# Optimization experiments

Measured on AMD Instinct MI355X. Metric: run time of the kernel, lower is better.

The kernel has to match this reference:

```python
import jax, jax.numpy as jnp
import numpy as np

H = 64
N_G, E_G = 30000, 60000
N_LG, E_LG = 60000, 60000


def setup_inputs() -> dict:
    key = jax.random.key(0)
    ks = jax.random.split(key, 30)
    rn = lambda k, s, sc=0.05: jax.random.normal(k, s, jnp.float32) * sc
    return {
        "gx": jax.random.normal(ks[0], (N_G, 20), jnp.float32),
        "g_edge_index": jax.random.randint(ks[1], (2, E_G), 0, N_G, jnp.int32),
        "g_edge_attr": jax.random.uniform(ks[2], (E_G, 4), dtype=jnp.float32),
        "lgx": jax.random.normal(ks[3], (N_LG, 5), jnp.float32),
        "lg_edge_index": jax.random.randint(ks[4], (2, E_LG), 0, N_LG, jnp.int32),
        "lg_edge_attr": jax.random.uniform(ks[5], (E_LG, 1), dtype=jnp.float32),
        "adduct": jax.random.normal(ks[6], (3,), jnp.float32),
        "lin0_w": rn(ks[7], (20, H)), "lin0_b": rn(ks[8], (H,)),
        "g_nn_w1": rn(ks[9], (4, H)), "g_nn_b1": rn(ks[10], (H,)),
        "g_nn_w2": rn(ks[11], (H, H * H), 0.01), "g_nn_b2": rn(ks[12], (H * H,), 0.01),
        "g_root": rn(ks[13], (H, H)), "g_bias": rn(ks[14], (H,)),
        "lin0_lg_w": rn(ks[15], (5, H)), "lin0_lg_b": rn(ks[16], (H,)),
        "lg_nn_w1": rn(ks[17], (1, H)), "lg_nn_b1": rn(ks[18], (H,)),
        "lg_nn_w2": rn(ks[19], (H, H * H), 0.01), "lg_nn_b2": rn(ks[20], (H * H,), 0.01),
        "lg_root": rn(ks[21], (H, H)), "lg_bias": rn(ks[22], (H,)),
        "bott_w": rn(ks[23], (H + H + 3, 384)), "bott_b": rn(ks[24], (384,)),
        "lin1_w": rn(ks[25], (384, 384)), "lin1_b": rn(ks[26], (384,)),
        "lin2_w": rn(ks[27], (384, 1)), "lin2_b": rn(ks[28], (1,)),
    }


def _ecc_branch(x_in, edge_index, edge_attr, w1, b1, w2, b2, root, bias, n_iters, num_nodes):
    """N iterations of NNConv(aggr='mean') + ReLU, then sum pool over nodes."""
    src, tgt = edge_index[0], edge_index[1]  # source->target flow (PyG default)
    # edge MLP -> per-edge [in, out] weight (edge_attr is loop-invariant, compute once)
    W = (jax.nn.relu(edge_attr @ w1 + b1) @ w2 + b2).reshape(-1, H, H)  # [E, H, H]
    cnt = jnp.maximum(
        jax.ops.segment_sum(jnp.ones((tgt.shape[0],), x_in.dtype), tgt, num_segments=num_nodes),
        1.0,
    )
    x = x_in
    for _ in range(n_iters):
        msg = jnp.einsum('ei,eio->eo', x[src], W)  # gather + batched matvec
        agg = jax.ops.segment_sum(msg, tgt, num_segments=num_nodes) / cnt[:, None]  # scatter-mean
        x = jax.nn.relu(x @ root + agg + bias)  # root transform + bias (NNConv defaults)
    return x.sum(axis=0)  # sum pooling -> [H]


def reference(gx, g_edge_index, g_edge_attr, lgx, lg_edge_index, lg_edge_attr, adduct,
              lin0_w, lin0_b, g_nn_w1, g_nn_b1, g_nn_w2, g_nn_b2, g_root, g_bias,
              lin0_lg_w, lin0_lg_b, lg_nn_w1, lg_nn_b1, lg_nn_w2, lg_nn_b2, lg_root, lg_bias,
              bott_w, bott_b, lin1_w, lin1_b, lin2_w, lin2_b):
    out_g = _ecc_branch(jax.nn.relu(gx @ lin0_w + lin0_b), g_edge_index, g_edge_attr,
                        g_nn_w1, g_nn_b1, g_nn_w2, g_nn_b2, g_root, g_bias, 3, N_G)
    out_lg = _ecc_branch(jax.nn.relu(lgx @ lin0_lg_w + lin0_lg_b), lg_edge_index, lg_edge_attr,
                         lg_nn_w1, lg_nn_b1, lg_nn_w2, lg_nn_b2, lg_root, lg_bias, 3, N_LG)
    out = jnp.concatenate([out_g, out_lg, adduct], axis=-1)  # [131]
    out = jax.nn.relu(out @ bott_w + bott_b)
    for _ in range(6):
        out = jax.nn.relu(out @ lin1_w + lin1_b)
    return out @ lin2_w + lin2_b  # [1]
```

## Files before the change

### kernel.cpp

```cpp
#include <hip/hip_runtime.h>

typedef unsigned short u16;
using short8_t  = __attribute__((ext_vector_type(8)))  short;
using float16_t = __attribute__((ext_vector_type(16))) float;
using float2v   = __attribute__((ext_vector_type(2)))  float;

#define NKT 260
#define DEG_CAP 32

__device__ __forceinline__ float bf2f(u16 b) { return __uint_as_float(((unsigned)b) << 16); }
__device__ __forceinline__ u16 f2bf(float f) {
  unsigned u = __float_as_uint(f);
  return (u16)((u + 0x7fffu + ((u >> 16) & 1u)) >> 16);
}

union U8 { short8_t s; uint4 v; unsigned u[4]; };

__device__ __forceinline__ short8_t scale8r(U8 xr, float2v h2) {
  U8 out;
  #pragma unroll
  for (int p = 0; p < 4; ++p) {
    float2v r;
    r[0] = __uint_as_float(xr.u[p] << 16);
    r[1] = __uint_as_float(xr.u[p] & 0xffff0000u);
    r = r * h2;
    out.u[p] = __builtin_amdgcn_perm(__float_as_uint(r[1]), __float_as_uint(r[0]), 0x07060302);
  }
  return out.s;
}

template<int IN>
__device__ __forceinline__ void affine_body(
    const float* __restrict__ Xin, const float* __restrict__ W, const float* __restrict__ Bv,
    u16* __restrict__ Xout, int N, int gid)
{
  int n = gid >> 6, o = gid & 63;
  if (n >= N) return;
  float acc = Bv[o];
  #pragma unroll
  for (int i = 0; i < IN; ++i)
    acc = fmaf(Xin[n * IN + i], W[i * 64 + o], acc);
  Xout[gid] = f2bf(fmaxf(acc, 0.f));
}

__global__ __launch_bounds__(256) void affine_all_kernel(
    const float* __restrict__ gx, const float* __restrict__ l0w, const float* __restrict__ l0b, u16* __restrict__ xg,
    const float* __restrict__ lgx, const float* __restrict__ llw, const float* __restrict__ llb, u16* __restrict__ xl,
    const float* __restrict__ gea, const float* __restrict__ gw1, const float* __restrict__ gb1, u16* __restrict__ hg,
    const float* __restrict__ lea, const float* __restrict__ lw1, const float* __restrict__ lb1, u16* __restrict__ hl,
    int B0, int B1, int B2, int B3, int NG, int NLG, int EG, int ELG,
    int* __restrict__ zero_ptr, int NZ)
{
  int b = blockIdx.x, t = threadIdx.x;
  if (b < B0)       affine_body<20>(gx, l0w, l0b, xg, NG, b * 256 + t);
  else if (b < B1)  affine_body<5>(lgx, llw, llb, xl, NLG, (b - B0) * 256 + t);
  else if (b < B2)  affine_body<4>(gea, gw1, gb1, hg, EG, (b - B1) * 256 + t);
  else if (b < B3)  affine_body<1>(lea, lw1, lb1, hl, ELG, (b - B2) * 256 + t);
  else {
    int idx = (b - B3) * 256 + t;
    if (idx < NZ) zero_ptr[idx] = 0;
  }
}

__device__ __forceinline__ void bpack_body(
    const float* __restrict__ w2, const float* __restrict__ b2, u16* __restrict__ Bp, int gid)
{
  if (gid >= NKT * 128) return;
  int lane = gid & 63;
  int nt = (gid >> 6) & 1;
  int kt = gid >> 7;
  int o = nt * 32 + (lane & 31);
  int kbase = kt * 16 + (lane >> 5) * 8;
  u16 vals[8];
  #pragma unroll
  for (int j = 0; j < 8; ++j) {
    int k = kbase + j;
    vals[j] = f2bf((k < 4096) ? w2[(k >> 6) * 4096 + (k & 63) * 64 + o]
                              : b2[(k - 4096) * 64 + o]);
  }
  uint4 pack;
  pack.x = (unsigned)vals[0] | ((unsigned)vals[1] << 16);
  pack.y = (unsigned)vals[2] | ((unsigned)vals[3] << 16);
  pack.z = (unsigned)vals[4] | ((unsigned)vals[5] << 16);
  pack.w = (unsigned)vals[6] | ((unsigned)vals[7] << 16);
  *(uint4*)(Bp + (size_t)gid * 8) = pack;
}

__device__ __forceinline__ void rootpack_body(const float* __restrict__ root, u16* __restrict__ Rp, int gid)
{
  if (gid >= 512) return;
  int lane = gid & 63;
  int nt = (gid >> 6) & 1;
  int kt = gid >> 7;
  int o = nt * 32 + (lane & 31);
  int kbase = kt * 16 + (lane >> 5) * 8;
  u16 vals[8];
  #pragma unroll
  for (int j = 0; j < 8; ++j) vals[j] = f2bf(root[(kbase + j) * 64 + o]);
  uint4 pack;
  pack.x = (unsigned)vals[0] | ((unsigned)vals[1] << 16);
  pack.y = (unsigned)vals[2] | ((unsigned)vals[3] << 16);
  pack.z = (unsigned)vals[4] | ((unsigned)vals[5] << 16);
  pack.w = (unsigned)vals[6] | ((unsigned)vals[7] << 16);
  *(uint4*)(Rp + (size_t)gid * 8) = pack;
}

__global__ __launch_bounds__(256) void pack_all_kernel(
    const float* __restrict__ gw2, const float* __restrict__ gb2, u16* __restrict__ bpg,
    const float* __restrict__ lw2, const float* __restrict__ lb2, u16* __restrict__ bpl,
    const float* __restrict__ groot, u16* __restrict__ rpg,
    const float* __restrict__ lroot, u16* __restrict__ rpl)
{
  int b = blockIdx.x, t = threadIdx.x;
  if (b < 130)       bpack_body(gw2, gb2, bpg, b * 256 + t);
  else if (b < 260)  bpack_body(lw2, lb2, bpl, (b - 130) * 256 + t);
  else if (b < 262)  rootpack_body(groot, rpg, (b - 260) * 256 + t);
  else               rootpack_body(lroot, rpl, (b - 262) * 256 + t);
}

__device__ __forceinline__ void hist_body(
    const int* __restrict__ eidx, int* __restrict__ cnt, int* __restrict__ elist, int E, int e)
{
  if (e < E) {
    int tg = eidx[E + e];
    int pos = atomicAdd(cnt + tg, 1);
    if (pos < DEG_CAP) elist[(size_t)tg * DEG_CAP + pos] = e;
  }
}

__global__ __launch_bounds__(256) void hist_kernel(
    const int* __restrict__ eig, int* __restrict__ cg, int* __restrict__ elg, int Eg, int nbg,
    const int* __restrict__ eil, int* __restrict__ cl, int* __restrict__ ell, int El)
{
  int b = blockIdx.x, t = threadIdx.x;
  if (b < nbg) hist_body(eig, cg, elg, Eg, b * 256 + t);
  else         hist_body(eil, cl, ell, El, (b - nbg) * 256 + t);
}

__global__ __launch_bounds__(256, 2) void msg_gemm_kernel(
    const u16* __restrict__ Xg, const u16* __restrict__ Hg, const u16* __restrict__ Bg,
    const int* __restrict__ eig, u16* __restrict__ Mg, int Eg, int nbg,
    const u16* __restrict__ Xl, const u16* __restrict__ Hl, const u16* __restrict__ Bl,
    const int* __restrict__ eil, u16* __restrict__ Ml, int El)
{
  __shared__ __align__(16) u16 sB[4][8192];

  const int b = blockIdx.x;
  const u16 *X, *Hh, *Bp; const int* eidx; u16* msg; int E, e0;
  if (b < nbg) { X = Xg; Hh = Hg; Bp = Bg; eidx = eig; msg = Mg; E = Eg; e0 = b * 256; }
  else         { X = Xl; Hh = Hl; Bp = Bl; eidx = eil; msg = Ml; E = El; e0 = (b - nbg) * 256; }

  const int t = threadIdx.x;
  const int lane = t & 63;
  const int wid = t >> 6;
  const int ml = lane & 31;
  const int q  = lane >> 5;

  #pragma unroll
  for (int c0 = 0; c0 < 3; ++c0) {
    const u16* src = Bp + (size_t)c0 * 8192 + (size_t)wid * 2048 + (size_t)lane * 8;
    u16* dst = &sB[c0][wid * 2048];
    #pragma unroll
    for (int d = 0; d < 4; ++d)
      __builtin_amdgcn_global_load_lds((const __attribute__((address_space(1))) void*)(src + d * 512),
                                       (__attribute__((address_space(3))) void*)(dst + d * 512), 16, 0, 0);
  }

  const int ea  = e0 + wid * 64 + ml;
  const int eb  = ea + 32;
  const int eac = ea < E ? ea : E - 1;
  const int ebc = eb < E ? eb : E - 1;
  const int sa  = eidx[eac], sb = eidx[ebc];

  U8 xra[4], xrb[4];
  {
    const u16* xpa = X + (size_t)sa * 64 + q * 8;
    const u16* xpb = X + (size_t)sb * 64 + q * 8;
    #pragma unroll
    for (int s = 0; s < 4; ++s) {
      xra[s].v = *(const uint4*)(xpa + s * 16);
      xrb[s].v = *(const uint4*)(xpb + s * 16);
    }
  }

  const uint4* ha4 = (const uint4*)(Hh + (size_t)eac * 64);
  const uint4* hb4 = (const uint4*)(Hh + (size_t)ebc * 64);
  uint4 hc0 = ha4[0], hn0 = ha4[1];
  uint4 hc1 = hb4[0], hn1 = hb4[1];

  float16_t acc00, acc01, acc10, acc11;
  #pragma unroll
  for (int i = 0; i < 16; ++i) { acc00[i] = 0.f; acc01[i] = 0.f; acc10[i] = 0.f; acc11[i] = 0.f; }

  const u16* bsrc = Bp + (size_t)3 * 8192 + (size_t)wid * 2048 + (size_t)lane * 8;

  const short8_t* sb8 = (const short8_t*)&sB[0][0];

  asm volatile("s_waitcnt vmcnt(0)" ::: "memory");
  __builtin_amdgcn_sched_barrier(0);
  __builtin_amdgcn_s_barrier();

  for (int g = 0; g < 8; ++g) {
    #pragma unroll
    for (int cc = 0; cc < 4; ++cc) {
      {
        #pragma unroll
        for (int d = 0; d < 4; ++d)
          __builtin_amdgcn_global_load_lds((const __attribute__((address_space(1))) void*)(bsrc + d * 512),
                                           (__attribute__((address_space(3))) void*)(&sB[(cc + 3) & 3][wid * 2048] + d * 512), 16, 0, 0);
        bsrc += 8192;
      }
      unsigned w0 = ((const unsigned*)&hc0)[cc];
      unsigned w1 = ((const unsigned*)&hc1)[cc];
      const int sbase = (cc & 3) * 1024;
      #pragma unroll
      for (int hh = 0; hh < 2; ++hh) {
        float2v h20, h21;
        h20[0] = h20[1] = bf2f((u16)(hh ? (w0 >> 16) : (w0 & 0xffffu)));
        h21[0] = h21[1] = bf2f((u16)(hh ? (w1 >> 16) : (w1 & 0xffffu)));
        #pragma unroll
        for (int tt = 0; tt < 4; ++tt) {
          short8_t b0 = sb8[sbase + (hh * 4 + tt) * 128 + lane];
          short8_t b1 = sb8[sbase + (hh * 4 + tt) * 128 + 64 + lane];
          short8_t a0 = scale8r(xra[tt], h20);
          short8_t a1 = scale8r(xrb[tt], h21);
          acc00 = __builtin_amdgcn_mfma_f32_32x32x16_bf16(a0, b0, acc00, 0, 0, 0);
          acc01 = __builtin_amdgcn_mfma_f32_32x32x16_bf16(a0, b1, acc01, 0, 0, 0);
          acc10 = __builtin_amdgcn_mfma_f32_32x32x16_bf16(a1, b0, acc10, 0, 0, 0);
          acc11 = __builtin_amdgcn_mfma_f32_32x32x16_bf16(a1, b1, acc11, 0, 0, 0);
        }
      }
      asm volatile("s_waitcnt lgkmcnt(0)" ::: "memory");
      asm volatile("s_waitcnt vmcnt(8)" ::: "memory");
      __builtin_amdgcn_sched_barrier(0);
      __builtin_amdgcn_s_barrier();
    }
    hc0 = hn0; hc1 = hn1;
    if (g < 6) { hn0 = ha4[g + 2]; hn1 = hb4[g + 2]; }
  }

  {
    float2v h2; h2[0] = 1.0f; h2[1] = 1.0f;
    #pragma unroll
    for (int tt = 0; tt < 4; ++tt) {
      short8_t b0 = sb8[tt * 128 + lane];
      short8_t b1 = sb8[tt * 128 + 64 + lane];
      short8_t a0 = scale8r(xra[tt], h2);
      short8_t a1 = scale8r(xrb[tt], h2);
      acc00 = __builtin_amdgcn_mfma_f32_32x32x16_bf16(a0, b0, acc00, 0, 0, 0);
      acc01 = __builtin_amdgcn_mfma_f32_32x32x16_bf16(a0, b1, acc01, 0, 0, 0);
      acc10 = __builtin_amdgcn_mfma_f32_32x32x16_bf16(a1, b0, acc10, 0, 0, 0);
      acc11 = __builtin_amdgcn_mfma_f32_32x32x16_bf16(a1, b1, acc11, 0, 0, 0);
    }
  }

  #pragma unroll
  for (int reg = 0; reg < 16; ++reg) {
    int row = (reg & 3) + 8 * (reg >> 2) + 4 * q;
    int e1 = e0 + wid * 64 + row;
    int e2 = e1 + 32;
    if (e1 < E) {
      msg[(size_t)e1 * 64 + ml]      = f2bf(acc00[reg]);
      msg[(size_t)e1 * 64 + 32 + ml] = f2bf(acc01[reg]);
    }
    if (e2 < E) {
      msg[(size_t)e2 * 64 + ml]      = f2bf(acc10[reg]);
      msg[(size_t)e2 * 64 + 32 + ml] = f2bf(acc11[reg]);
    }
  }
}

__global__ __launch_bounds__(256, 4) void update_kernel(
    const u16* __restrict__ Xig, const u16* __restrict__ Mgg, const int* __restrict__ cg,
    const int* __restrict__ elg, const u16* __restrict__ rpg, const float* __restrict__ bg,
    u16* __restrict__ Xog, int Ng, int nbg,
    const u16* __restrict__ Xil, const u16* __restrict__ Mgl, const int* __restrict__ cl,
    const int* __restrict__ ell, const u16* __restrict__ rpl, const float* __restrict__ bl,
    u16* __restrict__ Xol, int Nl)
{
  const int b = blockIdx.x;
  const u16 *Xin, *rootp, *msg; const float *bias; const int *cnt, *elist;
  u16* Xout; int N, n0;
  if (b < nbg) { Xin=Xig; msg=Mgg; cnt=cg; elist=elg; rootp=rpg; bias=bg; Xout=Xog; N=Ng; n0=b*128; }
  else         { Xin=Xil; msg=Mgl; cnt=cl; elist=ell; rootp=rpl; bias=bl; Xout=Xol; N=Nl; n0=(b-nbg)*128; }

  const int t = threadIdx.x;
  const int lane = t & 63;
  const int wid = t >> 6;
  const int ml = lane & 31;
  const int q  = lane >> 5;
  const int nbase = n0 + wid * 32;

  const int na = nbase + ml;
  const int nac = na < N ? na : N - 1;

  U8 xr[4];
  {
    const u16* xp = Xin + (size_t)nac * 64 + q * 8;
    #pragma unroll
    for (int s = 0; s < 4; ++s) xr[s].v = *(const uint4*)(xp + s * 16);
  }
  U8 rp[8];
  {
    const uint4* rpv = (const uint4*)rootp;
    #pragma unroll
    for (int i = 0; i < 8; ++i) rp[i].v = rpv[i * 64 + lane];
  }
  const float bias0 = bias[ml], bias1 = bias[32 + ml];

  float16_t acc0, acc1;
  #pragma unroll
  for (int i = 0; i < 16; ++i) { acc0[i] = 0.f; acc1[i] = 0.f; }
  #pragma unroll
  for (int kt = 0; kt < 4; ++kt) {
    acc0 = __builtin_amdgcn_mfma_f32_32x32x16_bf16(xr[kt].s, rp[kt * 2 + 0].s, acc0, 0, 0, 0);
    acc1 = __builtin_amdgcn_mfma_f32_32x32x16_bf16(xr[kt].s, rp[kt * 2 + 1].s, acc1, 0, 0, 0);
  }

  #pragma unroll
  for (int reg = 0; reg < 16; ++reg) {
    int row = (reg & 3) + 8 * (reg >> 2) + 4 * q;
    int nn = nbase + row;
    if (nn < N) {
      int c = cnt[nn];
      int cc = c < DEG_CAP ? c : DEG_CAP;
      const int* ep = elist + (size_t)nn * DEG_CAP;
      float a0 = 0.f, a1 = 0.f;
      int j = 0;
      for (; j + 4 <= cc; j += 4) {
        int e0i = ep[j], e1i = ep[j + 1], e2i = ep[j + 2], e3i = ep[j + 3];
        u16 m00 = msg[(size_t)e0i * 64 + ml], m01 = msg[(size_t)e0i * 64 + 32 + ml];
        u16 m10 = msg[(size_t)e1i * 64 + ml], m11 = msg[(size_t)e1i * 64 + 32 + ml];
        u16 m20 = msg[(size_t)e2i * 64 + ml], m21 = msg[(size_t)e2i * 64 + 32 + ml];
        u16 m30 = msg[(size_t)e3i * 64 + ml], m31 = msg[(size_t)e3i * 64 + 32 + ml];
        a0 += bf2f(m00) + bf2f(m10) + bf2f(m20) + bf2f(m30);
        a1 += bf2f(m01) + bf2f(m11) + bf2f(m21) + bf2f(m31);
      }
      for (; j < cc; ++j) {
        int e = ep[j];
        a0 += bf2f(msg[(size_t)e * 64 + ml]);
        a1 += bf2f(msg[(size_t)e * 64 + 32 + ml]);
      }
      float rc = (c > 1) ? (1.0f / (float)c) : 1.0f;
      float o0 = fmaxf(acc0[reg] + a0 * rc + bias0, 0.f);
      float o1 = fmaxf(acc1[reg] + a1 * rc + bias1, 0.f);
      Xout[(size_t)nn * 64 + ml]      = f2bf(o0);
      Xout[(size_t)nn * 64 + 32 + ml] = f2bf(o1);
    }
  }
}

__device__ __forceinline__ void pool_body(const u16* __restrict__ X, float* __restrict__ part,
                                          int nchunks, int bid, int t)
{
  __shared__ float red[64];
  if (t < 64) red[t] = 0.f;
  __syncthreads();
  int gid = bid * 256 + t;
  float s[8];
  #pragma unroll
  for (int j = 0; j < 8; ++j) s[j] = 0.f;
  for (int i = gid; i < nchunks; i += 256 * 256) {
    uint4 v = ((const uint4*)X)[i];
    s[0] += bf2f((u16)(v.x & 0xffffu)); s[1] += bf2f((u16)(v.x >> 16));
    s[2] += bf2f((u16)(v.y & 0xffffu)); s[3] += bf2f((u16)(v.y >> 16));
    s[4] += bf2f((u16)(v.z & 0xffffu)); s[5] += bf2f((u16)(v.z >> 16));
    s[6] += bf2f((u16)(v.w & 0xffffu)); s[7] += bf2f((u16)(v.w >> 16));
  }
  int cg = (gid & 7) * 8;
  #pragma unroll
  for (int j = 0; j < 8; ++j) atomicAdd(red + cg + j, s[j]);
  __syncthreads();
  if (t < 64) part[bid * 64 + t] = red[t];
}

__global__ __launch_bounds__(256) void pool_kernel(
    const u16* __restrict__ Xg, float* __restrict__ pg_part, int ncg,
    const u16* __restrict__ Xl, float* __restrict__ pl_part, int ncl)
{
  int b = blockIdx.x, t = threadIdx.x;
  if (b < 256) pool_body(Xg, pg_part, ncg, b, t);
  else         pool_body(Xl, pl_part, ncl, b - 256, t);
}

__global__ __launch_bounds__(768) void head_kernel(
    const float* __restrict__ ppg, const float* __restrict__ ppl, const float* __restrict__ adduct,
    const float* __restrict__ bw, const float* __restrict__ bb,
    const float* __restrict__ l1w, const float* __restrict__ l1b,
    const float* __restrict__ l2w, const float* __restrict__ l2b,
    float* __restrict__ out)
{
  __shared__ float hv[384];
  __shared__ float u[384];
  __shared__ float ph[2][384];
  __shared__ float wred[6];
  const int t = threadIdx.x;
  const int col  = (t < 384) ? t : t - 384;
  const int half = (t < 384) ? 0 : 1;

  if (t < 384) hv[t] = 0.f;
  __syncthreads();

  {
    const int cg = t & 15, br = (t >> 4) & 1, tb = t >> 5;
    const float* pp = br ? ppl : ppg;
    float a0 = 0.f, a1 = 0.f, a2 = 0.f, a3 = 0.f;
    for (int b = tb; b < 256; b += 24) {
      const float4 v = *(const float4*)(pp + b * 64 + cg * 4);
      a0 += v.x; a1 += v.y; a2 += v.z; a3 += v.w;
    }
    float* dst = hv + br * 64 + cg * 4;
    atomicAdd(dst + 0, a0); atomicAdd(dst + 1, a1);
    atomicAdd(dst + 2, a2); atomicAdd(dst + 3, a3);
    if (t < 3) hv[128 + t] = adduct[t];
  }
  __syncthreads();

  {
    const int i0 = half ? 66 : 0;
    const int i1 = half ? 131 : 66;
    float pa[8];
    #pragma unroll
    for (int j = 0; j < 8; ++j) pa[j] = 0.f;
    int i = i0;
    for (; i + 8 <= i1; i += 8) {
      #pragma unroll
      for (int j = 0; j < 8; ++j)
        pa[j] = fmaf(hv[i + j], bw[(i + j) * 384 + col], pa[j]);
    }
    for (; i < i1; ++i) pa[0] = fmaf(hv[i], bw[i * 384 + col], pa[0]);
    float s = ((pa[0] + pa[1]) + (pa[2] + pa[3])) + ((pa[4] + pa[5]) + (pa[6] + pa[7]));
    ph[half][col] = s;
  }
  __syncthreads();
  if (t < 384) u[t] = fmaxf(bb[t] + ph[0][t] + ph[1][t], 0.f);
  __syncthreads();

  for (int L = 0; L < 6; ++L) {
    const int i0 = half * 192;
    float pa[16];
    #pragma unroll
    for (int j = 0; j < 16; ++j) pa[j] = 0.f;
    #pragma unroll 1
    for (int i = i0; i < i0 + 192; i += 16) {
      #pragma unroll
      for (int j = 0; j < 16; ++j)
        pa[j] = fmaf(u[i + j], l1w[(i + j) * 384 + col], pa[j]);
    }
    float s = (((pa[0] + pa[1]) + (pa[2] + pa[3])) + ((pa[4] + pa[5]) + (pa[6] + pa[7])))
            + (((pa[8] + pa[9]) + (pa[10] + pa[11])) + ((pa[12] + pa[13]) + (pa[14] + pa[15])));
    ph[half][col] = s;
    __syncthreads();
    if (t < 384) u[t] = fmaxf(l1b[t] + ph[0][t] + ph[1][t], 0.f);
    __syncthreads();
  }

  {
    if (t < 384) {
      float p = u[t] * l2w[t];
      #pragma unroll
      for (int off = 32; off > 0; off >>= 1) p += __shfl_down(p, off);
      if ((t & 63) == 0) wred[t >> 6] = p;
    }
    __syncthreads();
    if (t == 0) {
      float s = l2b[0];
      #pragma unroll
      for (int i = 0; i < 6; ++i) s += wred[i];
      out[0] = s;
    }
  }
}

extern "C" void kernel_launch(void* const* d_in, const int* in_sizes, int n_in,
                              void* d_out, int out_size, void* d_ws, size_t ws_size,
                              hipStream_t stream)
{
  const int NG = 30000, EG = 60000, NLG = 60000, ELG = 60000;

  const float* gx      = (const float*)d_in[0];
  const int*   g_ei    = (const int*)  d_in[1];
  const float* g_ea    = (const float*)d_in[2];
  const float* lgx     = (const float*)d_in[3];
  const int*   lg_ei   = (const int*)  d_in[4];
  const float* lg_ea   = (const float*)d_in[5];
  const float* adduct  = (const float*)d_in[6];
  const float* lin0_w  = (const float*)d_in[7];
  const float* lin0_b  = (const float*)d_in[8];
  const float* g_w1    = (const float*)d_in[9];
  const float* g_b1    = (const float*)d_in[10];
  const float* g_w2    = (const float*)d_in[11];
  const float* g_b2    = (const float*)d_in[12];
  const float* g_root  = (const float*)d_in[13];
  const float* g_bias  = (const float*)d_in[14];
  const float* l0lg_w  = (const float*)d_in[15];
  const float* l0lg_b  = (const float*)d_in[16];
  const float* lg_w1   = (const float*)d_in[17];
  const float* lg_b1   = (const float*)d_in[18];
  const float* lg_w2   = (const float*)d_in[19];
  const float* lg_b2   = (const float*)d_in[20];
  const float* lg_root = (const float*)d_in[21];
  const float* lg_bias = (const float*)d_in[22];
  const float* bott_w  = (const float*)d_in[23];
  const float* bott_b  = (const float*)d_in[24];
  const float* lin1_w  = (const float*)d_in[25];
  const float* lin1_b  = (const float*)d_in[26];
  const float* lin2_w  = (const float*)d_in[27];
  const float* lin2_b  = (const float*)d_in[28];

  char* p = (char*)d_ws;
  auto alloc = [&](size_t bytes) { char* r = p; p += (bytes + 255) & ~(size_t)255; return r; };
  u16*   xg_a   = (u16*)  alloc((size_t)NG  * 64 * 2);
  u16*   xg_b   = (u16*)  alloc((size_t)NG  * 64 * 2);
  u16*   xl_a   = (u16*)  alloc((size_t)NLG * 64 * 2);
  u16*   xl_b   = (u16*)  alloc((size_t)NLG * 64 * 2);
  u16*   h_g    = (u16*)  alloc((size_t)EG  * 64 * 2);
  u16*   h_l    = (u16*)  alloc((size_t)ELG * 64 * 2);
  u16*   bp_g   = (u16*)  alloc((size_t)NKT * 128 * 8 * 2 + 49152);
  u16*   bp_l   = (u16*)  alloc((size_t)NKT * 128 * 8 * 2 + 49152);
  u16*   rp_g   = (u16*)  alloc(512 * 8 * 2);
  u16*   rp_l   = (u16*)  alloc(512 * 8 * 2);
  u16*   msg_g  = (u16*)  alloc((size_t)EG  * 64 * 2);
  u16*   msg_l  = (u16*)  alloc((size_t)ELG * 64 * 2);
  int*   cnt_g  = (int*)  alloc((size_t)NG  * 4);
  int*   cnt_l  = (int*)  alloc((size_t)NLG * 4);
  int*   el_g   = (int*)  alloc((size_t)NG  * DEG_CAP * 4);
  int*   el_l   = (int*)  alloc((size_t)NLG * DEG_CAP * 4);
  float* pp_g   = (float*)alloc(256 * 64 * 4);
  float* pp_l   = (float*)alloc(256 * 64 * 4);

  const int B0 = NG * 64 / 256, B1 = B0 + NLG * 64 / 256, B2 = B1 + EG * 64 / 256;
  const int B3 = B2 + ELG * 64 / 256;
  const int NZ = (int)(((size_t)((char*)cnt_l - (char*)cnt_g)) / 4) + NLG;
  const int zb = (NZ + 255) / 256;
  affine_all_kernel<<<B3 + zb, 256, 0, stream>>>(
      gx, lin0_w, lin0_b, xg_a, lgx, l0lg_w, l0lg_b, xl_a,
      g_ea, g_w1, g_b1, h_g, lg_ea, lg_w1, lg_b1, h_l,
      B0, B1, B2, B3, NG, NLG, EG, ELG, cnt_g, NZ);
  pack_all_kernel<<<264, 256, 0, stream>>>(g_w2, g_b2, bp_g, lg_w2, lg_b2, bp_l,
                                           g_root, rp_g, lg_root, rp_l);
  const int nhg = (EG + 255) / 256, nhl = (ELG + 255) / 256;
  hist_kernel<<<nhg + nhl, 256, 0, stream>>>(g_ei, cnt_g, el_g, EG, nhg, lg_ei, cnt_l, el_l, ELG);

  const int nbg_m = (EG + 255) / 256, nbl_m = (ELG + 255) / 256;
  const int nbg_u = (NG + 127) / 128, nbl_u = (NLG + 127) / 128;
  u16 *xgc = xg_a, *xgn = xg_b, *xlc = xl_a, *xln = xl_b;
  for (int it = 0; it < 3; ++it) {
    msg_gemm_kernel<<<nbg_m + nbl_m, 256, 0, stream>>>(
        xgc, h_g, bp_g, g_ei, msg_g, EG, nbg_m,
        xlc, h_l, bp_l, lg_ei, msg_l, ELG);
    update_kernel<<<nbg_u + nbl_u, 256, 0, stream>>>(
        xgc, msg_g, cnt_g, el_g, rp_g, g_bias, xgn, NG, nbg_u,
        xlc, msg_l, cnt_l, el_l, rp_l, lg_bias, xln, NLG);
    u16* tmp = xgc; xgc = xgn; xgn = tmp;
    tmp = xlc; xlc = xln; xln = tmp;
  }

  pool_kernel<<<512, 256, 0, stream>>>(xgc, pp_g, NG * 8, xlc, pp_l, NLG * 8);

  head_kernel<<<1, 768, 0, stream>>>(pp_g, pp_l, adduct,
                                     bott_w, bott_b, lin1_w, lin1_b, lin2_w, lin2_b,
                                     (float*)d_out);
}
```

Before: 501.6 us.

## Prefetch head weights into L2 during pooling and cache lin1 rows in registers

Adds 64 extra blocks to the pool kernel that read bott_w and lin1_w so those weights are resident in cache before the single-block head kernel starts. The head kernel also loads 128 of each thread's 192 lin1_w values into registers once and reuses them across all six layers, so only the remaining 64 rows are reread from memory per layer. The aim is to cut the latency-bound weight reloads in the serial head MLP. The cost is heavy register pressure at 768 threads per block, which may cause spills, and the prefetch adds memory traffic to the pool kernel.

Result: slower. 578.6 us (+15.4%).

```diff
diff --git a/kernel.cpp b/kernel.cpp
--- a/kernel.cpp
+++ b/kernel.cpp
@@ -374,13 +374,37 @@
   if (t < 64) part[bid * 64 + t] = red[t];
 }
 
+__device__ __forceinline__ void prefetch_body(const float* __restrict__ bw,
+                                              const float* __restrict__ l1w, int pb, int t)
+{
+  const int chunk = pb >> 3;
+  float acc = 0.f;
+  {
+    const float4* p = (const float4*)bw;
+    for (int i = chunk * 1572 + t; i < (chunk + 1) * 1572; i += 256) {
+      float4 v = p[i];
+      acc += v.x + v.y + v.z + v.w;
+    }
+  }
+  {
+    const float4* p = (const float4*)l1w;
+    for (int i = chunk * 4608 + t; i < (chunk + 1) * 4608; i += 256) {
+      float4 v = p[i];
+      acc += v.x + v.y + v.z + v.w;
+    }
+  }
+  asm volatile("" :: "v"(acc));
+}
+
 __global__ __launch_bounds__(256) void pool_kernel(
     const u16* __restrict__ Xg, float* __restrict__ pg_part, int ncg,
-    const u16* __restrict__ Xl, float* __restrict__ pl_part, int ncl)
+    const u16* __restrict__ Xl, float* __restrict__ pl_part, int ncl,
+    const float* __restrict__ bw, const float* __restrict__ l1w)
 {
   int b = blockIdx.x, t = threadIdx.x;
-  if (b < 256) pool_body(Xg, pg_part, ncg, b, t);
-  else         pool_body(Xl, pl_part, ncl, b - 256, t);
+  if (b < 256)      pool_body(Xg, pg_part, ncg, b, t);
+  else if (b < 512) pool_body(Xl, pl_part, ncl, b - 256, t);
+  else              prefetch_body(bw, l1w, b - 512, t);
 }
 
 __global__ __launch_bounds__(768) void head_kernel(
@@ -390,15 +414,21 @@
     const float* __restrict__ l2w, const float* __restrict__ l2b,
     float* __restrict__ out)
 {
-  __shared__ float hv[384];
+  __shared__ float hv[132];
   __shared__ float u[384];
   __shared__ float ph[2][384];
   __shared__ float wred[6];
   const int t = threadIdx.x;
   const int col  = (t < 384) ? t : t - 384;
   const int half = (t < 384) ? 0 : 1;
-
-  if (t < 384) hv[t] = 0.f;
+  const int i0 = half * 192;
+
+  float wc[128];
+  #pragma unroll
+  for (int j = 0; j < 128; ++j)
+    wc[j] = l1w[(i0 + j) * 384 + col];
+
+  if (t < 132) hv[t] = 0.f;
   __syncthreads();
 
   {
@@ -417,18 +447,18 @@
   __syncthreads();
 
   {
-    const int i0 = half ? 66 : 0;
-    const int i1 = half ? 131 : 66;
+    const int b0 = half ? 66 : 0;
+    const int b1 = half ? 131 : 66;
     float pa[8];
     #pragma unroll
     for (int j = 0; j < 8; ++j) pa[j] = 0.f;
-    int i = i0;
-    for (; i + 8 <= i1; i += 8) {
+    int i = b0;
+    for (; i + 8 <= b1; i += 8) {
       #pragma unroll
       for (int j = 0; j < 8; ++j)
         pa[j] = fmaf(hv[i + j], bw[(i + j) * 384 + col], pa[j]);
     }
-    for (; i < i1; ++i) pa[0] = fmaf(hv[i], bw[i * 384 + col], pa[0]);
+    for (; i < b1; ++i) pa[0] = fmaf(hv[i], bw[i * 384 + col], pa[0]);
     float s = ((pa[0] + pa[1]) + (pa[2] + pa[3])) + ((pa[4] + pa[5]) + (pa[6] + pa[7]));
     ph[half][col] = s;
   }
@@ -437,18 +467,23 @@
   __syncthreads();
 
   for (int L = 0; L < 6; ++L) {
-    const int i0 = half * 192;
-    float pa[16];
-    #pragma unroll
-    for (int j = 0; j < 16; ++j) pa[j] = 0.f;
+    float pa[8];
+    #pragma unroll
+    for (int j = 0; j < 8; ++j) pa[j] = 0.f;
+    #pragma unroll
+    for (int j = 0; j < 128; ++j)
+      pa[j & 7] = fmaf(u[i0 + j], wc[j], pa[j & 7]);
+    float pb[8];
+    #pragma unroll
+    for (int j = 0; j < 8; ++j) pb[j] = 0.f;
     #pragma unroll 1
-    for (int i = i0; i < i0 + 192; i += 16) {
+    for (int jb = 128; jb < 192; jb += 8) {
       #pragma unroll
-      for (int j = 0; j < 16; ++j)
-        pa[j] = fmaf(u[i + j], l1w[(i + j) * 384 + col], pa[j]);
+      for (int k = 0; k < 8; ++k)
+        pb[k] = fmaf(u[i0 + jb + k], l1w[(i0 + jb + k) * 384 + col], pb[k]);
     }
     float s = (((pa[0] + pa[1]) + (pa[2] + pa[3])) + ((pa[4] + pa[5]) + (pa[6] + pa[7])))
-            + (((pa[8] + pa[9]) + (pa[10] + pa[11])) + ((pa[12] + pa[13]) + (pa[14] + pa[15])));
+            + (((pb[0] + pb[1]) + (pb[2] + pb[3])) + ((pb[4] + pb[5]) + (pb[6] + pb[7])));
     ph[half][col] = s;
     __syncthreads();
     if (t < 384) u[t] = fmaxf(l1b[t] + ph[0][t] + ph[1][t], 0.f);
@@ -556,7 +591,8 @@
     tmp = xlc; xlc = xln; xln = tmp;
   }
 
-  pool_kernel<<<512, 256, 0, stream>>>(xgc, pp_g, NG * 8, xlc, pp_l, NLG * 8);
+  pool_kernel<<<576, 256, 0, stream>>>(xgc, pp_g, NG * 8, xlc, pp_l, NLG * 8,
+                                       bott_w, lin1_w);
 
   head_kernel<<<1, 768, 0, stream>>>(pp_g, pp_l, adduct,
                                      bott_w, bott_b, lin1_w, lin1_b, lin2_w, lin2_b,
```
